# Kernel tuning notes

Hardware: AMD Instinct MI355X
Metric: run time of the kernel (lower is better)

## Reference

```python
import jax, jax.numpy as jnp
import numpy as np

TWO_PI = 2.0 * np.pi
EPS = 1e-8

def diff_round(x):
    # differentiable rounding used throughout the repo
    return x - jnp.sin(TWO_PI * x) / TWO_PI

def harder_diff_round(x):
    return diff_round(diff_round(x))

def differentiable_eq(a, b):
    a = harder_diff_round(a)
    b = harder_diff_round(b)
    return harder_diff_round(a * b + (1 - a) * (1 - b))

def differentiable_and(a, b):
    return diff_round(a) * diff_round(b)

def filter_mask_of_intrest(mask, mid):
    # mask: [D, D, 4], mid: [4]
    agree = differentiable_eq(mask, mid[None, None, :])  # [D, D, 4]
    a = differentiable_and(agree[..., 0], agree[..., 1])
    b = differentiable_and(agree[..., 2], agree[..., 3])
    return differentiable_and(a, b)  # [D, D]

def translate_in_axis(m, axis, is_forward):
    # shift by 1 with zero padding, matching jnp.take + jnp.pad in source
    D0, D1 = m.shape
    if axis == 0:
        if is_forward:
            return jnp.pad(m[:-1, :], ((1, 0), (0, 0)))
        return jnp.pad(m[1:, :], ((0, 1), (0, 0)))
    else:
        if is_forward:
            return jnp.pad(m[:, :-1], ((0, 0), (1, 0)))
        return jnp.pad(m[:, 1:], ((0, 0), (0, 1)))

def eq_simpl(a, b):
    return a * b + (1 - a) * (1 - b)

def or_simple(a, b):
    return a * b + (1 - a) * a + (1 - b) * a

def soft_erode_around(prev, curr, nxt, up, down):
    edge_diff = 1 - eq_simpl(prev, nxt)
    edge_diff_ud = 1 - eq_simpl(up, down)
    s0a = edge_diff * curr
    s0b = edge_diff_ud * curr
    should_be_0 = or_simple(s0a, s0b)
    return (1 - should_be_0) * curr

def get_eroded_mask(a):
    a_b = translate_in_axis(a, 0, 0)
    a_f = translate_in_axis(a, 0, 1)
    a_u = translate_in_axis(a, 1, 0)
    a_d = translate_in_axis(a, 1, 1)
    return soft_erode_around(a_b, a, a_f, a_u, a_d)

def _apply_on_single_area(img, mask, mid, edge):
    # img: [D,D,1], mask: [D,D,4], mid: [4], edge: [D,D]
    mc = filter_mask_of_intrest(mask, mid)        # [D,D]
    eroded = get_eroded_mask(mc)                  # [D,D]
    masked_edges = eroded * edge                  # [D,D]
    mc1 = mc[..., None]                           # [D,D,1]
    masked_image = mc1 * img                      # [D,D,1]
    loss = jnp.mean(masked_edges)
    denom = jnp.sum(mc1) + EPS
    meann = jnp.sum(masked_image) / denom
    varr = jnp.sum(((masked_image - meann) * mc1) ** 2) / denom
    return masked_edges[..., None], varr * loss * 1000.0

def setup_inputs() -> dict:
    key = jax.random.key(0)
    k0, k1, k2, k3 = jax.random.split(key, 4)
    B, A, D, C = 2, 8192, 16, 4
    resized_image = jax.random.uniform(k0, (B, A, D, D, 1), jnp.float32)
    mask_combined = jax.random.uniform(k1, (B, A, D, D, C), jnp.float32)
    initial_mask_id = jnp.round(jax.random.uniform(k2, (B, A, C), jnp.float32))
    edge_map = jax.random.uniform(k3, (B, A, D, D), jnp.float32)
    return {"resized_image": resized_image, "mask_combined": mask_combined,
            "initial_mask_id": initial_mask_id, "edge_map": edge_map}

def reference(resized_image, mask_combined, initial_mask_id, edge_map):
    f = jax.vmap(jax.vmap(_apply_on_single_area))  # over batch, then areas
    return f(resized_image, mask_combined, initial_mask_id, edge_map)
```

## Files before the change

### kernel.cpp

```cpp
#include <hip/hip_runtime.h>

#define INV_TWO_PI_F 0.15915494309189533577f

__device__ __forceinline__ float dround(float x) {
    return __builtin_fmaf(__builtin_amdgcn_sinf(x), -INV_TWO_PI_F, x);
}

__global__ void __launch_bounds__(256, 8)
deconv_area_kernel(const float* __restrict__ img,
                   const float* __restrict__ mask,
                   const float* __restrict__ mid,
                   const float* __restrict__ edge,
                   float* __restrict__ out_edges,
                   float* __restrict__ out_scalar)
{
    const int wid = blockIdx.x * 4 + (threadIdx.x >> 6);
    const int t   = threadIdx.x & 63;
    const size_t p = (size_t)wid;

    const float4 im4 = reinterpret_cast<const float4*>(img )[p * 64 + t];
    const float4 ed4 = reinterpret_cast<const float4*>(edge)[p * 64 + t];
    const float4* mk = reinterpret_cast<const float4*>(mask) + p * 256 + 4 * t;
    const float4 mm0 = mk[0], mm1 = mk[1], mm2 = mk[2], mm3 = mk[3];
    const float4 md  = reinterpret_cast<const float4*>(mid)[p];

    const bool h0 = md.x > 0.5f;
    const bool h1 = md.y > 0.5f;
    const bool h2 = md.z > 0.5f;
    const bool h3 = md.w > 0.5f;

    const float imv[4] = {im4.x, im4.y, im4.z, im4.w};
    const float edv[4] = {ed4.x, ed4.y, ed4.z, ed4.w};
    const float4 mm[4] = {mm0, mm1, mm2, mm3};

    float mc[4], mi[4];
    #pragma unroll
    for (int k = 0; k < 4; ++k) {
        float w0 = mm[k].x, w1 = mm[k].y, w2 = mm[k].z, w3 = mm[k].w;
        #pragma unroll
        for (int r = 0; r < 5; ++r) {
            w0 = dround(w0); w1 = dround(w1); w2 = dround(w2); w3 = dround(w3);
        }
        const float da0 = h0 ? w0 : 1.0f - w0;
        const float da1 = h1 ? w1 : 1.0f - w1;
        const float da2 = h2 ? w2 : 1.0f - w2;
        const float da3 = h3 ? w3 : 1.0f - w3;
        mc[k] = dround(da0 * da1) * dround(da2 * da3);
        mi[k] = mc[k] * imv[k];
    }

    float s1 = mc[0] + mc[1] + mc[2] + mc[3];
    float s2 = mi[0] + mi[1] + mi[2] + mi[3];
    #pragma unroll
    for (int m = 1; m < 64; m <<= 1) {
        s1 += __shfl_xor(s1, m);
        s2 += __shfl_xor(s2, m);
    }
    const float inv_d = __builtin_amdgcn_rcpf(s1 + 1e-8f);
    const float meann = s2 * inv_d;

    float pr[4], nr[4];
    #pragma unroll
    for (int k = 0; k < 4; ++k) {
        const float u = __shfl_up(mc[k], 4);
        const float d = __shfl_down(mc[k], 4);
        pr[k] = (t >= 4)  ? u : 0.0f;
        nr[k] = (t < 60) ? d : 0.0f;
    }
    const float lEdge = __shfl_up(mc[3], 1);
    const float rEdge = __shfl_down(mc[0], 1);
    float lf[4], rt[4];
    lf[0] = ((t & 3) > 0) ? lEdge : 0.0f;
    lf[1] = mc[0]; lf[2] = mc[1]; lf[3] = mc[2];
    rt[3] = ((t & 3) < 3) ? rEdge : 0.0f;
    rt[0] = mc[1]; rt[1] = mc[2]; rt[2] = mc[3];

    float me[4];
    float r1 = 0.0f, r2 = 0.0f;
    #pragma unroll
    for (int k = 0; k < 4; ++k) {
        const float ed_fb = 1.0f - (nr[k] * pr[k] + (1.0f - nr[k]) * (1.0f - pr[k]));
        const float ed_ud = 1.0f - (rt[k] * lf[k] + (1.0f - rt[k]) * (1.0f - lf[k]));
        const float s0a = ed_fb * mc[k];
        const float s0b = ed_ud * mc[k];
        const float sb0 = s0a * s0b + (1.0f - s0a) * s0a + (1.0f - s0b) * s0a;
        me[k] = (1.0f - sb0) * mc[k] * edv[k];
        const float vv = (mi[k] - meann) * mc[k];
        r1 += vv * vv;
        r2 += me[k];
    }

    float4 o;
    o.x = me[0]; o.y = me[1]; o.z = me[2]; o.w = me[3];
    reinterpret_cast<float4*>(out_edges)[p * 64 + t] = o;

    #pragma unroll
    for (int m = 1; m < 64; m <<= 1) {
        r1 += __shfl_xor(r1, m);
        r2 += __shfl_xor(r2, m);
    }
    if (t == 0) {
        const float varr = r1 * inv_d;
        const float loss = r2 * (1.0f / 256.0f);
        out_scalar[p] = varr * loss * 1000.0f;
    }
}

extern "C" void kernel_launch(void* const* d_in, const int* in_sizes, int n_in,
                              void* d_out, int out_size, void* d_ws, size_t ws_size,
                              hipStream_t stream)
{
    const float* img  = (const float*)d_in[0];
    const float* mask = (const float*)d_in[1];
    const float* mid  = (const float*)d_in[2];
    const float* edge = (const float*)d_in[3];

    const int n_areas = in_sizes[3] / 256;

    float* out0 = (float*)d_out;
    float* out1 = (float*)d_out + (size_t)n_areas * 256;

    deconv_area_kernel<<<dim3(n_areas / 4), dim3(256), 0, stream>>>(
        img, mask, mid, edge, out0, out1);
}
```

Before: 24.24 us.

## Switch per-thread pixel mapping to strided layout for coalesced loads and stores

```diff
diff --git a/kernel.cpp b/kernel.cpp
--- a/kernel.cpp
+++ b/kernel.cpp
@@ -18,19 +18,26 @@
     const int t   = threadIdx.x & 63;
     const size_t p = (size_t)wid;
 
-    const float4 im4 = reinterpret_cast<const float4*>(img )[p * 64 + t];
-    const float4 ed4 = reinterpret_cast<const float4*>(edge)[p * 64 + t];
-    const float4* mk = reinterpret_cast<const float4*>(mask) + p * 256 + 4 * t;
-    const float4 mm0 = mk[0], mm1 = mk[1], mm2 = mk[2], mm3 = mk[3];
-    const float4 md  = reinterpret_cast<const float4*>(mid)[p];
+    const float4* maskv = reinterpret_cast<const float4*>(mask) + p * 256;
+    const float4 mm0 = maskv[t];
+    const float4 mm1 = maskv[t + 64];
+    const float4 mm2 = maskv[t + 128];
+    const float4 mm3 = maskv[t + 192];
+    const float* imgp  = img  + p * 256;
+    const float* edgep = edge + p * 256;
+    float imv[4], edv[4];
+    #pragma unroll
+    for (int k = 0; k < 4; ++k) {
+        imv[k] = imgp [t + 64 * k];
+        edv[k] = edgep[t + 64 * k];
+    }
+    const float4 md = reinterpret_cast<const float4*>(mid)[p];
 
     const bool h0 = md.x > 0.5f;
     const bool h1 = md.y > 0.5f;
     const bool h2 = md.z > 0.5f;
     const bool h3 = md.w > 0.5f;
 
-    const float imv[4] = {im4.x, im4.y, im4.z, im4.w};
-    const float edv[4] = {ed4.x, ed4.y, ed4.z, ed4.w};
     const float4 mm[4] = {mm0, mm1, mm2, mm3};
 
     float mc[4], mi[4];
@@ -59,21 +66,20 @@
     const float inv_d = __builtin_amdgcn_rcpf(s1 + 1e-8f);
     const float meann = s2 * inv_d;
 
-    float pr[4], nr[4];
+    float pr[4], nr[4], lf[4], rt[4];
     #pragma unroll
     for (int k = 0; k < 4; ++k) {
-        const float u = __shfl_up(mc[k], 4);
-        const float d = __shfl_down(mc[k], 4);
-        pr[k] = (t >= 4)  ? u : 0.0f;
-        nr[k] = (t < 60) ? d : 0.0f;
+        const float up16 = __shfl_up(mc[k], 16);
+        const float dn16 = __shfl_down(mc[k], 16);
+        const float prWrap = (k > 0) ? __shfl_down(mc[k - 1], 48) : 0.0f;
+        const float nrWrap = (k < 3) ? __shfl_up(mc[k + 1], 48) : 0.0f;
+        pr[k] = (t >= 16) ? up16 : prWrap;
+        nr[k] = (t <  48) ? dn16 : nrWrap;
+        const float l1 = __shfl_up(mc[k], 1);
+        const float r1_ = __shfl_down(mc[k], 1);
+        lf[k] = ((t & 15) > 0)  ? l1  : 0.0f;
+        rt[k] = ((t & 15) < 15) ? r1_ : 0.0f;
     }
-    const float lEdge = __shfl_up(mc[3], 1);
-    const float rEdge = __shfl_down(mc[0], 1);
-    float lf[4], rt[4];
-    lf[0] = ((t & 3) > 0) ? lEdge : 0.0f;
-    lf[1] = mc[0]; lf[2] = mc[1]; lf[3] = mc[2];
-    rt[3] = ((t & 3) < 3) ? rEdge : 0.0f;
-    rt[0] = mc[1]; rt[1] = mc[2]; rt[2] = mc[3];
 
     float me[4];
     float r1 = 0.0f, r2 = 0.0f;
@@ -90,9 +96,9 @@
         r2 += me[k];
     }
 
-    float4 o;
-    o.x = me[0]; o.y = me[1]; o.z = me[2]; o.w = me[3];
-    reinterpret_cast<float4*>(out_edges)[p * 64 + t] = o;
+    float* outp = out_edges + p * 256;
+    #pragma unroll
+    for (int k = 0; k < 4; ++k) outp[t + 64 * k] = me[k];
 
     #pragma unroll
     for (int m = 1; m < 64; m <<= 1) {
```

After: 24.79 us. 2.3% more time.

## Process four areas per wave with double-buffered register prefetch

Applied to the files above, without the earlier changes.

```diff
diff --git a/kernel.cpp b/kernel.cpp
--- a/kernel.cpp
+++ b/kernel.cpp
@@ -6,32 +6,36 @@
     return __builtin_fmaf(__builtin_amdgcn_sinf(x), -INV_TWO_PI_F, x);
 }
 
-__global__ void __launch_bounds__(256, 8)
-deconv_area_kernel(const float* __restrict__ img,
-                   const float* __restrict__ mask,
-                   const float* __restrict__ mid,
-                   const float* __restrict__ edge,
-                   float* __restrict__ out_edges,
-                   float* __restrict__ out_scalar)
+struct AreaData {
+    float4 im, ed, m0, m1, m2, m3, md;
+};
+
+__device__ __forceinline__ AreaData load_area(
+    const float* __restrict__ img, const float* __restrict__ mask,
+    const float* __restrict__ mid, const float* __restrict__ edge,
+    size_t p, int t)
 {
-    const int wid = blockIdx.x * 4 + (threadIdx.x >> 6);
-    const int t   = threadIdx.x & 63;
-    const size_t p = (size_t)wid;
+    AreaData a;
+    a.im = reinterpret_cast<const float4*>(img )[p * 64 + t];
+    a.ed = reinterpret_cast<const float4*>(edge)[p * 64 + t];
+    const float4* mk = reinterpret_cast<const float4*>(mask) + p * 256 + 4 * t;
+    a.m0 = mk[0]; a.m1 = mk[1]; a.m2 = mk[2]; a.m3 = mk[3];
+    a.md = reinterpret_cast<const float4*>(mid)[p];
+    return a;
+}
 
-    const float4 im4 = reinterpret_cast<const float4*>(img )[p * 64 + t];
-    const float4 ed4 = reinterpret_cast<const float4*>(edge)[p * 64 + t];
-    const float4* mk = reinterpret_cast<const float4*>(mask) + p * 256 + 4 * t;
-    const float4 mm0 = mk[0], mm1 = mk[1], mm2 = mk[2], mm3 = mk[3];
-    const float4 md  = reinterpret_cast<const float4*>(mid)[p];
+__device__ __forceinline__ void process_area(
+    const AreaData& A, const size_t p, const int t,
+    float* __restrict__ out_edges, float* __restrict__ out_scalar)
+{
+    const bool h0 = A.md.x > 0.5f;
+    const bool h1 = A.md.y > 0.5f;
+    const bool h2 = A.md.z > 0.5f;
+    const bool h3 = A.md.w > 0.5f;
 
-    const bool h0 = md.x > 0.5f;
-    const bool h1 = md.y > 0.5f;
-    const bool h2 = md.z > 0.5f;
-    const bool h3 = md.w > 0.5f;
-
-    const float imv[4] = {im4.x, im4.y, im4.z, im4.w};
-    const float edv[4] = {ed4.x, ed4.y, ed4.z, ed4.w};
-    const float4 mm[4] = {mm0, mm1, mm2, mm3};
+    const float imv[4] = {A.im.x, A.im.y, A.im.z, A.im.w};
+    const float edv[4] = {A.ed.x, A.ed.y, A.ed.z, A.ed.w};
+    const float4 mm[4] = {A.m0, A.m1, A.m2, A.m3};
 
     float mc[4], mi[4];
     #pragma unroll
@@ -106,6 +110,34 @@
     }
 }
 
+__global__ void __launch_bounds__(256, 4)
+deconv_area_kernel(const float* __restrict__ img,
+                   const float* __restrict__ mask,
+                   const float* __restrict__ mid,
+                   const float* __restrict__ edge,
+                   float* __restrict__ out_edges,
+                   float* __restrict__ out_scalar,
+                   int n_waves)
+{
+    const int w = blockIdx.x * 4 + (threadIdx.x >> 6);
+    const int t = threadIdx.x & 63;
+    const size_t NW = (size_t)n_waves;
+
+    const size_t p0 = (size_t)w;
+    const size_t p1 = p0 + NW;
+    const size_t p2 = p1 + NW;
+    const size_t p3 = p2 + NW;
+
+    AreaData A = load_area(img, mask, mid, edge, p0, t);
+    AreaData B = load_area(img, mask, mid, edge, p1, t);
+    process_area(A, p0, t, out_edges, out_scalar);
+    A = load_area(img, mask, mid, edge, p2, t);
+    process_area(B, p1, t, out_edges, out_scalar);
+    B = load_area(img, mask, mid, edge, p3, t);
+    process_area(A, p2, t, out_edges, out_scalar);
+    process_area(B, p3, t, out_edges, out_scalar);
+}
+
 extern "C" void kernel_launch(void* const* d_in, const int* in_sizes, int n_in,
                               void* d_out, int out_size, void* d_ws, size_t ws_size,
                               hipStream_t stream)
@@ -116,10 +148,12 @@
     const float* edge = (const float*)d_in[3];
 
     const int n_areas = in_sizes[3] / 256;
+    const int n_waves = n_areas / 4;
+    const int n_blocks = n_waves / 4;
 
     float* out0 = (float*)d_out;
     float* out1 = (float*)d_out + (size_t)n_areas * 256;
 
-    deconv_area_kernel<<<dim3(n_areas / 4), dim3(256), 0, stream>>>(
-        img, mask, mid, edge, out0, out1);
+    deconv_area_kernel<<<dim3(n_blocks), dim3(256), 0, stream>>>(
+        img, mask, mid, edge, out0, out1, n_waves);
 }
```

Result: slower. 25.28 us (+4.3%).
